# Performance work log

Measured on AMD Instinct MI355X. Metric: run time of the kernel, lower is better.

The kernel has to match this reference:

```python
import jax, jax.numpy as jnp
import numpy as np

EMBED_DIM = 1024
NUM_HEADS = 16
HEAD_DIM = EMBED_DIM // NUM_HEADS
SCALING = HEAD_DIM ** (-0.5)
BSZ, SEQ = 2, 2048


def setup_inputs() -> dict:
    key = jax.random.key(0)
    ks = jax.random.split(key, 12)
    s = 1.0 / np.sqrt(EMBED_DIM)
    query = jax.random.normal(ks[0], (BSZ, SEQ, EMBED_DIM), dtype=jnp.float32)
    return {
        "query": query,
        "key": query,
        "value": query,
        "attn_bias": jax.random.normal(ks[1], (BSZ, NUM_HEADS, SEQ, SEQ), dtype=jnp.float32) * 0.1,
        "Wq": jax.random.normal(ks[2], (EMBED_DIM, EMBED_DIM), dtype=jnp.float32) * s,
        "bq": jax.random.normal(ks[3], (EMBED_DIM,), dtype=jnp.float32) * 0.01,
        "Wk": jax.random.normal(ks[4], (EMBED_DIM, EMBED_DIM), dtype=jnp.float32) * s,
        "bk": jax.random.normal(ks[5], (EMBED_DIM,), dtype=jnp.float32) * 0.01,
        "Wv": jax.random.normal(ks[6], (EMBED_DIM, EMBED_DIM), dtype=jnp.float32) * s,
        "bv": jax.random.normal(ks[7], (EMBED_DIM,), dtype=jnp.float32) * 0.01,
        "Wo": jax.random.normal(ks[8], (EMBED_DIM, EMBED_DIM), dtype=jnp.float32) * s,
        "bo": jax.random.normal(ks[9], (EMBED_DIM,), dtype=jnp.float32) * 0.01,
    }


def reference(query, key, value, attn_bias, Wq, bq, Wk, bk, Wv, bv, Wo, bo):
    # Self-attention: k and v are computed from `query` (key/value args ignored
    # by the original module). torch Linear: y = x @ W.T + b
    B, T, E = query.shape
    H, D = NUM_HEADS, HEAD_DIM
    q = (query @ Wq.T + bq) * SCALING
    k = query @ Wk.T + bk
    v = query @ Wv.T + bv
    # [B, T, H, D]
    q = q.reshape(B, T, H, D)
    k = k.reshape(B, T, H, D)
    v = v.reshape(B, T, H, D)
    # scores: [B, H, T, T]
    scores = jnp.einsum("bthd,bshd->bhts", q, k) + attn_bias
    probs = jax.nn.softmax(scores, axis=-1)
    # attention output: [B, T, H, D] -> [B, T, E]
    attn = jnp.einsum("bhts,bshd->bthd", probs, v).reshape(B, T, E)
    out = attn @ Wo.T + bo
    # need_weights=True default: average attention weights over heads [B, T, T]
    avg_weights = probs.mean(axis=1)
    return out, avg_weights
```

## Files before the change

kernel.cpp:

```cpp
#include <hip/hip_runtime.h>
#include <hip/hip_bf16.h>

#define B_ 2
#define H_ 16
#define T_ 2048
#define D_ 64
#define ED_ 1024

typedef __attribute__((ext_vector_type(8))) short bf16x8;
typedef __attribute__((ext_vector_type(4))) float f32x4;

__device__ __forceinline__ void gload16(const void* g, void* l) {
  __builtin_amdgcn_global_load_lds(
      (const __attribute__((address_space(1))) unsigned int*)(uintptr_t)g,
      (__attribute__((address_space(3))) unsigned int*)(uintptr_t)l,
      16, 0, 0);
}

__device__ __forceinline__ float b2f(short s) {
  unsigned int u = ((unsigned int)(unsigned short)s) << 16;
  return __builtin_bit_cast(float, u);
}

__global__ __launch_bounds__(256) void convert_f32_bf16(
    const float* __restrict__ x, const float* __restrict__ wq, const float* __restrict__ wk,
    const float* __restrict__ wv, const float* __restrict__ wo,
    __hip_bfloat16* __restrict__ xb, __hip_bfloat16* __restrict__ wqb,
    __hip_bfloat16* __restrict__ wkb, __hip_bfloat16* __restrict__ wvb,
    __hip_bfloat16* __restrict__ wob)
{
  int id = blockIdx.x * 256 + threadIdx.x;
  size_t e0 = (size_t)id * 4;
  const float* src; __hip_bfloat16* dst; size_t off;
  if (e0 < 4194304) { src = x; dst = xb; off = e0; }
  else {
    size_t r = e0 - 4194304;
    int wsel = (int)(r >> 20);
    off = r & 1048575;
    src = (wsel == 0) ? wq : (wsel == 1) ? wk : (wsel == 2) ? wv : wo;
    dst = (wsel == 0) ? wqb : (wsel == 1) ? wkb : (wsel == 2) ? wvb : wob;
  }
  float4 v = *(const float4*)(src + off);
  __hip_bfloat16 o[4];
  o[0] = __float2bfloat16(v.x); o[1] = __float2bfloat16(v.y);
  o[2] = __float2bfloat16(v.z); o[3] = __float2bfloat16(v.w);
  *(ushort4*)(dst + off) = *(ushort4*)o;
}

struct GemmP {
  const __hip_bfloat16* A;
  const __hip_bfloat16* Bw[3];
  const float* bias[3];
  void* out[3];
  float scale[3];
  int mode[3];
};

__global__ __launch_bounds__(256, 2) void gemm_nt(GemmP p)
{
  __shared__ __hip_bfloat16 As[128 * 64];
  __shared__ __hip_bfloat16 Bs[128 * 64];
  const int tid = threadIdx.x;
  const int z = blockIdx.z;
  const __hip_bfloat16* A = p.A;
  const __hip_bfloat16* Bw = p.Bw[z];
  const int bm0 = blockIdx.x * 128, bn0 = blockIdx.y * 128;
  const int l = tid & 63, w = tid >> 6;
  const int wr = w >> 1, wc = w & 1;
  const int lhi = l >> 4, llo = l & 15;
  const int swl = (llo & 7) << 3;

  f32x4 acc[4][4];
#pragma unroll
  for (int m = 0; m < 4; ++m)
#pragma unroll
    for (int n = 0; n < 4; ++n) acc[m][n] = (f32x4){0.f, 0.f, 0.f, 0.f};

  for (int kt = 0; kt < 1024; kt += 64) {
#pragma unroll
    for (int j = 0; j < 4; ++j) {
      int off = j * 2048 + tid * 8;
      int row = off >> 6;
      int col = off & 63;
      int cs = col ^ ((row & 7) << 3);
      gload16(&A[(size_t)(bm0 + row) * 1024 + kt + cs], &As[off]);
      gload16(&Bw[(size_t)(bn0 + row) * 1024 + kt + cs], &Bs[off]);
    }
    __syncthreads();
#pragma unroll
    for (int kk = 0; kk < 2; ++kk) {
      bf16x8 af[4], bf[4];
#pragma unroll
      for (int m = 0; m < 4; ++m)
        af[m] = *(const bf16x8*)&As[(wr * 64 + m * 16 + llo) * 64 + ((kk * 32 + lhi * 8) ^ swl)];
#pragma unroll
      for (int n = 0; n < 4; ++n)
        bf[n] = *(const bf16x8*)&Bs[(wc * 64 + n * 16 + llo) * 64 + ((kk * 32 + lhi * 8) ^ swl)];
#pragma unroll
      for (int m = 0; m < 4; ++m)
#pragma unroll
        for (int n = 0; n < 4; ++n)
          acc[m][n] = __builtin_amdgcn_mfma_f32_16x16x32_bf16(af[m], bf[n], acc[m][n], 0, 0, 0);
    }
    __syncthreads();
  }

  const float* bias = p.bias[z];
  const float scale = p.scale[z];
  const int mode = p.mode[z];
  float bv[4];
#pragma unroll
  for (int n = 0; n < 4; ++n) bv[n] = bias[bn0 + wc * 64 + n * 16 + llo];
#pragma unroll
  for (int m = 0; m < 4; ++m) {
    int rowb = bm0 + wr * 64 + m * 16 + lhi * 4;
#pragma unroll
    for (int n = 0; n < 4; ++n) {
      int col = bn0 + wc * 64 + n * 16 + llo;
#pragma unroll
      for (int r = 0; r < 4; ++r) {
        float v = (acc[m][n][r] + bv[n]) * scale;
        int row = rowb + r;
        if (mode == 0) {
          ((__hip_bfloat16*)p.out[z])[(size_t)row * 1024 + col] = __float2bfloat16(v);
        } else if (mode == 1) {
          ((float*)p.out[z])[(size_t)row * 1024 + col] = v;
        } else {
          int bb = row >> 11, t = row & 2047;
          int hh = col >> 6, d = col & 63;
          ((__hip_bfloat16*)p.out[z])[((size_t)((bb * 16 + hh) * 64 + d)) * 2048 + t] =
              __float2bfloat16(v);
        }
      }
    }
  }
}

__global__ __launch_bounds__(256, 2) void attn_fwd(
    const __hip_bfloat16* __restrict__ qb,
    const __hip_bfloat16* __restrict__ kb,
    const __hip_bfloat16* __restrict__ vT,
    const float* __restrict__ bias,
    unsigned char* __restrict__ Ebuf,
    float* __restrict__ invl,
    __hip_bfloat16* __restrict__ attn)
{
  __shared__ __hip_bfloat16 Ks[2][64 * 64];
  __shared__ __hip_bfloat16 Vs[2][64 * 64];
  __shared__ float          bS[2][64 * 64];
  __shared__ __hip_bfloat16 Ps[64 * 64];
  const int tid = threadIdx.x;
  const int l = tid & 63, w = tid >> 6;
  const int lhi = l >> 4, llo = l & 15;
  const int swl = (llo & 7) << 3;
  const int qt = blockIdx.x, h = blockIdx.y, b = blockIdx.z;
  const int t0 = qt * 64;
  const __hip_bfloat16* kbase = kb + ((size_t)b * 2048) * 1024 + h * 64;
  const __hip_bfloat16* vbase = vT + ((size_t)((b * 16 + h) * 64)) * 2048;
  const float* bbase = bias + (((size_t)(b * 16 + h)) * 2048 + t0) * 2048;
  unsigned char* ebase = Ebuf + (((size_t)(b * 16 + h)) * 2048 + t0) * 2048;

  bf16x8 qa[2];
#pragma unroll
  for (int kk = 0; kk < 2; ++kk)
    qa[kk] = *(const bf16x8*)&qb[((size_t)(b * 2048 + t0 + w * 16 + llo)) * 1024 +
                                 h * 64 + kk * 32 + lhi * 8];

  f32x4 acc_o[4];
#pragma unroll
  for (int f = 0; f < 4; ++f) acc_o[f] = (f32x4){0.f, 0.f, 0.f, 0.f};
  float lrun[4] = {0.f, 0.f, 0.f, 0.f};

  const int erl = w * 16 + (l >> 2), ec = (l & 3) << 4;
  const int esw = (erl & 7) << 3;

#define STAGE(BUF, S0)                                                         \
  do {                                                                         \
    _Pragma("unroll") for (int j2 = 0; j2 < 2; ++j2) {                         \
      int off = j2 * 2048 + tid * 8;                                           \
      int row = off >> 6, col = off & 63;                                      \
      int cs = col ^ ((row & 7) << 3);                                         \
      gload16(&kbase[(size_t)((S0) + row) * 1024 + cs], &Ks[BUF][off]);        \
      gload16(&vbase[(size_t)row * 2048 + (S0) + cs], &Vs[BUF][off]);          \
    }                                                                          \
    _Pragma("unroll") for (int j2 = 0; j2 < 4; ++j2) {                         \
      int off = j2 * 1024 + tid * 4;                                           \
      int row = off >> 6, col = off & 63;                                      \
      int cs = col ^ (((row >> 2) & 3) << 4);                                  \
      gload16(&bbase[(size_t)row * 2048 + (S0) + cs], &bS[BUF][off]);          \
    }                                                                          \
  } while (0)

  STAGE(0, 0);
  asm volatile("s_waitcnt vmcnt(0)" ::: "memory");
  __builtin_amdgcn_sched_barrier(0);
  __builtin_amdgcn_s_barrier();

  for (int it = 0; it < 32; ++it) {
    const int s0 = it * 64;
    const int cur = it & 1;

    if (it < 31) {
      STAGE(cur ^ 1, s0 + 64);
      asm volatile("s_waitcnt vmcnt(9)" ::: "memory");
    } else {
      asm volatile("s_waitcnt vmcnt(1)" ::: "memory");
    }
    __builtin_amdgcn_sched_barrier(0);
    __builtin_amdgcn_s_barrier();

    f32x4 sa[4];
#pragma unroll
    for (int f = 0; f < 4; ++f) sa[f] = (f32x4){0.f, 0.f, 0.f, 0.f};
#pragma unroll
    for (int kk = 0; kk < 2; ++kk) {
#pragma unroll
      for (int f = 0; f < 4; ++f) {
        bf16x8 kf = *(const bf16x8*)&Ks[cur][(f * 16 + llo) * 64 +
                                            ((kk * 32 + lhi * 8) ^ swl)];
        sa[f] = __builtin_amdgcn_mfma_f32_16x16x32_bf16(qa[kk], kf, sa[f], 0, 0, 0);
      }
    }
    float rsum[4] = {0.f, 0.f, 0.f, 0.f};
#pragma unroll
    for (int f = 0; f < 4; ++f) {
      int col = f * 16 + llo;
#pragma unroll
      for (int r = 0; r < 4; ++r) {
        int row = w * 16 + lhi * 4 + r;
        float s = sa[f][r] + bS[cur][row * 64 + (col ^ (lhi << 4))];
        float ev = __expf(s);
        rsum[r] += ev;
        Ps[row * 64 + (col ^ (((lhi * 4 + r) & 7) << 3))] = __float2bfloat16(ev);
      }
    }
#pragma unroll
    for (int r = 0; r < 4; ++r) {
      float v = rsum[r];
      v += __shfl_xor(v, 1); v += __shfl_xor(v, 2);
      v += __shfl_xor(v, 4); v += __shfl_xor(v, 8);
      lrun[r] += v;
    }
    {
      bf16x8 e0 = *(const bf16x8*)&Ps[erl * 64 + (ec ^ esw)];
      bf16x8 e1 = *(const bf16x8*)&Ps[erl * 64 + ((ec + 8) ^ esw)];
      unsigned int d4[4];
#pragma unroll
      for (int q = 0; q < 2; ++q) {
        int lo0 = __builtin_amdgcn_cvt_pk_fp8_f32(b2f(e0[4 * q]) * 0.0625f,
                                                  b2f(e0[4 * q + 1]) * 0.0625f, 0, 0);
        d4[q] = __builtin_amdgcn_cvt_pk_fp8_f32(b2f(e0[4 * q + 2]) * 0.0625f,
                                                b2f(e0[4 * q + 3]) * 0.0625f, lo0, 1);
        int lo1 = __builtin_amdgcn_cvt_pk_fp8_f32(b2f(e1[4 * q]) * 0.0625f,
                                                  b2f(e1[4 * q + 1]) * 0.0625f, 0, 0);
        d4[2 + q] = __builtin_amdgcn_cvt_pk_fp8_f32(b2f(e1[4 * q + 2]) * 0.0625f,
                                                    b2f(e1[4 * q + 3]) * 0.0625f, lo1, 1);
      }
      *(uint4*)&ebase[(size_t)erl * 2048 + s0 + ec] = make_uint4(d4[0], d4[1], d4[2], d4[3]);
    }
#pragma unroll
    for (int kk = 0; kk < 2; ++kk) {
      bf16x8 pa = *(const bf16x8*)&Ps[(w * 16 + llo) * 64 + ((kk * 32 + lhi * 8) ^ swl)];
#pragma unroll
      for (int f = 0; f < 4; ++f) {
        bf16x8 vf = *(const bf16x8*)&Vs[cur][(f * 16 + llo) * 64 +
                                            ((kk * 32 + lhi * 8) ^ swl)];
        acc_o[f] = __builtin_amdgcn_mfma_f32_16x16x32_bf16(pa, vf, acc_o[f], 0, 0, 0);
      }
    }
    asm volatile("s_waitcnt lgkmcnt(0)" ::: "memory");
    __builtin_amdgcn_sched_barrier(0);
    __builtin_amdgcn_s_barrier();
  }
#undef STAGE

  float inv[4];
#pragma unroll
  for (int r = 0; r < 4; ++r) inv[r] = 1.f / lrun[r];
#pragma unroll
  for (int f = 0; f < 4; ++f) {
    int d = f * 16 + llo;
#pragma unroll
    for (int r = 0; r < 4; ++r) {
      int t = t0 + w * 16 + lhi * 4 + r;
      attn[((size_t)(b * 2048 + t)) * 1024 + h * 64 + d] =
          __float2bfloat16(acc_o[f][r] * inv[r]);
    }
  }
  if (llo == 0) {
#pragma unroll
    for (int r = 0; r < 4; ++r)
      invl[((size_t)(b * 16 + h)) * 2048 + t0 + w * 16 + lhi * 4 + r] = inv[r];
  }
}

__global__ __launch_bounds__(256) void avgw_k(
    const unsigned char* __restrict__ Ebuf, const float* __restrict__ invl,
    float* __restrict__ outw)
{
  int c = blockIdx.x * 256 + threadIdx.x;
  int b = c >> 18;
  int rem = c & 262143;
  int t = rem >> 7;
  int s0 = (rem & 127) << 4;
  float acc[16];
#pragma unroll
  for (int i = 0; i < 16; ++i) acc[i] = 0.f;
#pragma unroll
  for (int hh = 0; hh < 16; ++hh) {
    float inv = invl[((size_t)(b * 16 + hh)) * 2048 + t];
    uint4 evv = *(const uint4*)&Ebuf[(((size_t)(b * 16 + hh)) * 2048 + t) * 2048 + s0];
    unsigned int dw[4] = {evv.x, evv.y, evv.z, evv.w};
#pragma unroll
    for (int q = 0; q < 4; ++q) {
      acc[q * 4 + 0] += __builtin_amdgcn_cvt_f32_fp8(dw[q], 0) * inv;
      acc[q * 4 + 1] += __builtin_amdgcn_cvt_f32_fp8(dw[q], 1) * inv;
      acc[q * 4 + 2] += __builtin_amdgcn_cvt_f32_fp8(dw[q], 2) * inv;
      acc[q * 4 + 3] += __builtin_amdgcn_cvt_f32_fp8(dw[q], 3) * inv;
    }
  }
  float* o = outw + ((size_t)(b * 2048 + t)) * 2048 + s0;
#pragma unroll
  for (int q = 0; q < 4; ++q)
    *(float4*)(o + q * 4) = make_float4(acc[q * 4], acc[q * 4 + 1], acc[q * 4 + 2], acc[q * 4 + 3]);
}

extern "C" void kernel_launch(void* const* d_in, const int* in_sizes, int n_in,
                              void* d_out, int out_size, void* d_ws, size_t ws_size,
                              hipStream_t stream) {
  const float* query     = (const float*)d_in[0];
  const float* attn_bias = (const float*)d_in[3];
  const float* Wq = (const float*)d_in[4];
  const float* bq = (const float*)d_in[5];
  const float* Wk = (const float*)d_in[6];
  const float* bk = (const float*)d_in[7];
  const float* Wv = (const float*)d_in[8];
  const float* bv = (const float*)d_in[9];
  const float* Wo = (const float*)d_in[10];
  const float* bo = (const float*)d_in[11];
  float* out = (float*)d_out;

  char* ws = (char*)d_ws;
  __hip_bfloat16* xb   = (__hip_bfloat16*)(ws + 0);
  __hip_bfloat16* wqb  = (__hip_bfloat16*)(ws + 8388608);
  __hip_bfloat16* wkb  = (__hip_bfloat16*)(ws + 10485760);
  __hip_bfloat16* wvb  = (__hip_bfloat16*)(ws + 12582912);
  __hip_bfloat16* wob  = (__hip_bfloat16*)(ws + 14680064);
  __hip_bfloat16* qbf  = (__hip_bfloat16*)(ws + 16777216);
  __hip_bfloat16* kbf  = (__hip_bfloat16*)(ws + 25165824);
  __hip_bfloat16* vTb  = (__hip_bfloat16*)(ws + 33554432);
  __hip_bfloat16* atnb = (__hip_bfloat16*)(ws + 41943040);
  float*          linv = (float*)(ws + 50331648);
  unsigned char*  Ebuf = (unsigned char*)(ws + 50593792);

  convert_f32_bf16<<<8192, 256, 0, stream>>>(query, Wq, Wk, Wv, Wo, xb, wqb, wkb, wvb, wob);

  GemmP gp{};
  gp.A = xb;
  gp.Bw[0] = wqb; gp.Bw[1] = wkb; gp.Bw[2] = wvb;
  gp.bias[0] = bq; gp.bias[1] = bk; gp.bias[2] = bv;
  gp.out[0] = qbf; gp.out[1] = kbf; gp.out[2] = vTb;
  gp.scale[0] = 0.125f; gp.scale[1] = 1.f; gp.scale[2] = 1.f;
  gp.mode[0] = 0; gp.mode[1] = 0; gp.mode[2] = 2;
  gemm_nt<<<dim3(32, 8, 3), 256, 0, stream>>>(gp);

  attn_fwd<<<dim3(32, 16, 2), 256, 0, stream>>>(qbf, kbf, vTb, attn_bias, Ebuf, linv, atnb);

  avgw_k<<<2048, 256, 0, stream>>>(Ebuf, linv, out + 4194304);

  GemmP go{};
  go.A = atnb;
  go.Bw[0] = wob; go.bias[0] = bo; go.out[0] = out;
  go.scale[0] = 1.f; go.mode[0] = 1;
  gemm_nt<<<dim3(32, 8, 1), 256, 0, stream>>>(go);
}
```

Baseline: 286.8 us.

## Transpose QK^T MFMA output so each lane holds contiguous score columns

Swaps the MFMA operand order so each lane owns a query row with four consecutive key columns. The bias tile then loads as one f32x4 vector, P is written as bf16x4, and the fp8 probabilities go straight to global memory from registers. This drops the separate Ps re-read and repack pass for the E buffer and shrinks the row-sum reduction to two shuffles. In exchange it changes the bias LDS swizzle and wait counts, adds a shuffle to redistribute the inverse row sums, and replaces the 16-byte global stores with narrower 4-byte stores.

```diff
diff --git a/kernel.cpp b/kernel.cpp
--- a/kernel.cpp
+++ b/kernel.cpp
@@ -8,6 +8,7 @@
 #define ED_ 1024
 
 typedef __attribute__((ext_vector_type(8))) short bf16x8;
+typedef __attribute__((ext_vector_type(4))) short bf16x4;
 typedef __attribute__((ext_vector_type(4))) float f32x4;
 
 __device__ __forceinline__ void gload16(const void* g, void* l) {
@@ -20,6 +21,9 @@
 __device__ __forceinline__ float b2f(short s) {
   unsigned int u = ((unsigned int)(unsigned short)s) << 16;
   return __builtin_bit_cast(float, u);
+}
+__device__ __forceinline__ short f2b(float v) {
+  return __builtin_bit_cast(short, __float2bfloat16(v));
 }
 
 __global__ __launch_bounds__(256) void convert_f32_bf16(
@@ -155,24 +159,22 @@
   const int swl = (llo & 7) << 3;
   const int qt = blockIdx.x, h = blockIdx.y, b = blockIdx.z;
   const int t0 = qt * 64;
+  const int tl = w * 16 + llo;
   const __hip_bfloat16* kbase = kb + ((size_t)b * 2048) * 1024 + h * 64;
   const __hip_bfloat16* vbase = vT + ((size_t)((b * 16 + h) * 64)) * 2048;
   const float* bbase = bias + (((size_t)(b * 16 + h)) * 2048 + t0) * 2048;
-  unsigned char* ebase = Ebuf + (((size_t)(b * 16 + h)) * 2048 + t0) * 2048;
+  unsigned char* erow = Ebuf + (((size_t)(b * 16 + h)) * 2048 + t0 + tl) * 2048;
 
   bf16x8 qa[2];
 #pragma unroll
   for (int kk = 0; kk < 2; ++kk)
-    qa[kk] = *(const bf16x8*)&qb[((size_t)(b * 2048 + t0 + w * 16 + llo)) * 1024 +
+    qa[kk] = *(const bf16x8*)&qb[((size_t)(b * 2048 + t0 + tl)) * 1024 +
                                  h * 64 + kk * 32 + lhi * 8];
 
   f32x4 acc_o[4];
 #pragma unroll
   for (int f = 0; f < 4; ++f) acc_o[f] = (f32x4){0.f, 0.f, 0.f, 0.f};
-  float lrun[4] = {0.f, 0.f, 0.f, 0.f};
-
-  const int erl = w * 16 + (l >> 2), ec = (l & 3) << 4;
-  const int esw = (erl & 7) << 3;
+  float lrun = 0.f;
 
 #define STAGE(BUF, S0)                                                         \
   do {                                                                         \
@@ -186,7 +188,7 @@
     _Pragma("unroll") for (int j2 = 0; j2 < 4; ++j2) {                         \
       int off = j2 * 1024 + tid * 4;                                           \
       int row = off >> 6, col = off & 63;                                      \
-      int cs = col ^ (((row >> 2) & 3) << 4);                                  \
+      int cs = col ^ ((row & 15) << 2);                                        \
       gload16(&bbase[(size_t)row * 2048 + (S0) + cs], &bS[BUF][off]);          \
     }                                                                          \
   } while (0)
@@ -202,9 +204,9 @@
 
     if (it < 31) {
       STAGE(cur ^ 1, s0 + 64);
-      asm volatile("s_waitcnt vmcnt(9)" ::: "memory");
+      asm volatile("s_waitcnt vmcnt(12)" ::: "memory");
     } else {
-      asm volatile("s_waitcnt vmcnt(1)" ::: "memory");
+      asm volatile("s_waitcnt vmcnt(4)" ::: "memory");
     }
     __builtin_amdgcn_sched_barrier(0);
     __builtin_amdgcn_s_barrier();
@@ -218,46 +220,30 @@
       for (int f = 0; f < 4; ++f) {
         bf16x8 kf = *(const bf16x8*)&Ks[cur][(f * 16 + llo) * 64 +
                                             ((kk * 32 + lhi * 8) ^ swl)];
-        sa[f] = __builtin_amdgcn_mfma_f32_16x16x32_bf16(qa[kk], kf, sa[f], 0, 0, 0);
+        sa[f] = __builtin_amdgcn_mfma_f32_16x16x32_bf16(kf, qa[kk], sa[f], 0, 0, 0);
       }
     }
-    float rsum[4] = {0.f, 0.f, 0.f, 0.f};
+    float rsum = 0.f;
 #pragma unroll
     for (int f = 0; f < 4; ++f) {
-      int col = f * 16 + llo;
+      f32x4 bb = *(const f32x4*)&bS[cur][tl * 64 + (((f * 4 + lhi) ^ llo) << 2)];
+      float ev[4];
 #pragma unroll
       for (int r = 0; r < 4; ++r) {
-        int row = w * 16 + lhi * 4 + r;
-        float s = sa[f][r] + bS[cur][row * 64 + (col ^ (lhi << 4))];
-        float ev = __expf(s);
-        rsum[r] += ev;
-        Ps[row * 64 + (col ^ (((lhi * 4 + r) & 7) << 3))] = __float2bfloat16(ev);
+        ev[r] = __expf(sa[f][r] + bb[r]);
+        rsum += ev[r];
       }
-    }
-#pragma unroll
-    for (int r = 0; r < 4; ++r) {
-      float v = rsum[r];
-      v += __shfl_xor(v, 1); v += __shfl_xor(v, 2);
-      v += __shfl_xor(v, 4); v += __shfl_xor(v, 8);
-      lrun[r] += v;
-    }
-    {
-      bf16x8 e0 = *(const bf16x8*)&Ps[erl * 64 + (ec ^ esw)];
-      bf16x8 e1 = *(const bf16x8*)&Ps[erl * 64 + ((ec + 8) ^ esw)];
-      unsigned int d4[4];
-#pragma unroll
-      for (int q = 0; q < 2; ++q) {
-        int lo0 = __builtin_amdgcn_cvt_pk_fp8_f32(b2f(e0[4 * q]) * 0.0625f,
-                                                  b2f(e0[4 * q + 1]) * 0.0625f, 0, 0);
-        d4[q] = __builtin_amdgcn_cvt_pk_fp8_f32(b2f(e0[4 * q + 2]) * 0.0625f,
-                                                b2f(e0[4 * q + 3]) * 0.0625f, lo0, 1);
-        int lo1 = __builtin_amdgcn_cvt_pk_fp8_f32(b2f(e1[4 * q]) * 0.0625f,
-                                                  b2f(e1[4 * q + 1]) * 0.0625f, 0, 0);
-        d4[2 + q] = __builtin_amdgcn_cvt_pk_fp8_f32(b2f(e1[4 * q + 2]) * 0.0625f,
-                                                    b2f(e1[4 * q + 3]) * 0.0625f, lo1, 1);
-      }
-      *(uint4*)&ebase[(size_t)erl * 2048 + s0 + ec] = make_uint4(d4[0], d4[1], d4[2], d4[3]);
-    }
+      bf16x4 pw;
+      pw[0] = f2b(ev[0]); pw[1] = f2b(ev[1]);
+      pw[2] = f2b(ev[2]); pw[3] = f2b(ev[3]);
+      *(bf16x4*)&Ps[tl * 64 + ((f * 16 + lhi * 4) ^ ((llo & 7) << 3))] = pw;
+      int e01 = __builtin_amdgcn_cvt_pk_fp8_f32(ev[0] * 0.0625f, ev[1] * 0.0625f, 0, 0);
+      int e = __builtin_amdgcn_cvt_pk_fp8_f32(ev[2] * 0.0625f, ev[3] * 0.0625f, e01, 1);
+      *(unsigned int*)&erow[s0 + f * 16 + lhi * 4] = (unsigned int)e;
+    }
+    rsum += __shfl_xor(rsum, 16);
+    rsum += __shfl_xor(rsum, 32);
+    lrun += rsum;
 #pragma unroll
     for (int kk = 0; kk < 2; ++kk) {
       bf16x8 pa = *(const bf16x8*)&Ps[(w * 16 + llo) * 64 + ((kk * 32 + lhi * 8) ^ swl)];
@@ -274,9 +260,10 @@
   }
 #undef STAGE
 
-  float inv[4];
-#pragma unroll
-  for (int r = 0; r < 4; ++r) inv[r] = 1.f / lrun[r];
+  float invs = 1.f / lrun;
+  float inv4[4];
+#pragma unroll
+  for (int r = 0; r < 4; ++r) inv4[r] = __shfl(invs, lhi * 4 + r);
 #pragma unroll
   for (int f = 0; f < 4; ++f) {
     int d = f * 16 + llo;
@@ -284,14 +271,11 @@
     for (int r = 0; r < 4; ++r) {
       int t = t0 + w * 16 + lhi * 4 + r;
       attn[((size_t)(b * 2048 + t)) * 1024 + h * 64 + d] =
-          __float2bfloat16(acc_o[f][r] * inv[r]);
-    }
-  }
-  if (llo == 0) {
-#pragma unroll
-    for (int r = 0; r < 4; ++r)
-      invl[((size_t)(b * 16 + h)) * 2048 + t0 + w * 16 + lhi * 4 + r] = inv[r];
-  }
+          __float2bfloat16(acc_o[f][r] * inv4[r]);
+    }
+  }
+  if (l < 16)
+    invl[((size_t)(b * 16 + h)) * 2048 + t0 + w * 16 + l] = invs;
 }
 
 __global__ __launch_bounds__(256) void avgw_k(
```

Result: no change. 285.0 us (-0.6%).
